# Kernel optimization log

Measured on AMD Instinct MI355X. Metric: run time of the kernel, lower is better.

Reference implementation:

```python
import jax, jax.numpy as jnp
import numpy as np

N_NODES = 50000
N_EDGES = 800000
IN_FT = 128
HID_FT = 64
EMB_FT = 128
NUM_LAYERS = 4
NEG_SLOP = 0.2


def setup_inputs() -> dict:
    key = jax.random.key(0)
    ks = jax.random.split(key, 16)
    x = jax.random.normal(ks[0], (N_NODES, IN_FT), dtype=jnp.float32)
    edge_index = jax.random.randint(ks[1], (2, N_EDGES), 0, N_NODES, dtype=jnp.int64)
    edge_weight = jax.random.uniform(ks[2], (N_EDGES,), dtype=jnp.float32)
    def lin(k, fin, fout):
        s = 1.0 / np.sqrt(fin)
        kw, kb = jax.random.split(k)
        W = jax.random.uniform(kw, (fin, fout), minval=-s, maxval=s, dtype=jnp.float32)
        b = jax.random.uniform(kb, (fout,), minval=-s, maxval=s, dtype=jnp.float32)
        return W, b
    W1, b1 = lin(ks[3], IN_FT, HID_FT)
    W2, b2 = lin(ks[4], HID_FT, HID_FT)
    W3, b3 = lin(ks[5], HID_FT, HID_FT)
    W4, b4 = lin(ks[6], HID_FT, HID_FT)
    Wh, bh = lin(ks[7], NUM_LAYERS * HID_FT, EMB_FT)
    return {"x": x, "edge_index": edge_index, "edge_weight": edge_weight,
            "W1": W1, "b1": b1, "W2": W2, "b2": b2, "W3": W3, "b3": b3,
            "W4": W4, "b4": b4, "Wh": Wh, "bh": bh}


def _gcn_no_norm(x, src, dst, ew, W, b):
    # GCNConv(add_self_loops=False, normalize=False): plain weighted scatter-add
    h = x @ W                                   # [N, F]
    msg = h[src] * ew[:, None]                  # gather over edges [E, F]
    return jax.ops.segment_sum(msg, dst, num_segments=N_NODES) + b


def _gcn_norm(x, src, dst, ew, W, b):
    # Default GCNConv: add self loops (weight 1) + symmetric normalization.
    deg = jax.ops.segment_sum(ew, dst, num_segments=N_NODES) + 1.0  # +1 self loop
    dinv = jnp.where(deg > 0, jax.lax.rsqrt(deg), 0.0)
    norm = dinv[src] * ew * dinv[dst]           # [E]
    h = x @ W
    agg = jax.ops.segment_sum(h[src] * norm[:, None], dst, num_segments=N_NODES)
    agg = agg + (dinv * dinv)[:, None] * h      # self-loop term
    return agg + b


def _forward(x, edge_index, edge_weight, W1, b1, W2, b2, W3, b3, W4, b4, Wh, bh):
    src, dst = edge_index[0], edge_index[1]
    lrelu = lambda v: jax.nn.leaky_relu(v, NEG_SLOP)
    outs = []
    h = lrelu(_gcn_no_norm(x, src, dst, edge_weight, W1, b1))
    outs.append(h)  # dropout is identity in deterministic reference
    for W, b in ((W2, b2), (W3, b3), (W4, b4)):
        h = lrelu(_gcn_norm(h, src, dst, edge_weight, W, b))
        outs.append(h)
    cat = jnp.concatenate(outs, axis=-1)        # [N, num_layers*HID_FT]
    return cat @ Wh + bh


def reference(x, edge_index, edge_weight, W1, b1, W2, b2, W3, b3, W4, b4, Wh, bh):
    return _forward(x, edge_index, edge_weight, W1, b1, W2, b2, W3, b3, W4, b4, Wh, bh)
```

## Files before the change

### kernel.cpp

```cpp
#include <hip/hip_runtime.h>
#include <hip/hip_bf16.h>

#define NEG_SLOP 0.2f
typedef unsigned long long ull;
typedef __attribute__((ext_vector_type(8))) short bf16x8;
typedef __attribute__((ext_vector_type(4))) float f32x4;

__device__ __forceinline__ float lrelu(float v) { return v > 0.0f ? v : NEG_SLOP * v; }

__device__ __forceinline__ float bf2f(unsigned short u) {
    union { unsigned int i; float f; } c; c.i = ((unsigned int)u) << 16; return c.f;
}
__device__ __forceinline__ unsigned short f2bf(float f) {
    union { float f; unsigned int i; } c; c.f = f;
    unsigned int r = c.i + 0x7FFF + ((c.i >> 16) & 1);
    return (unsigned short)(r >> 16);
}

__global__ void histo_kernel(const int* __restrict__ dst, const float* __restrict__ ew,
                             ull* __restrict__ packed, int* __restrict__ rank, int n_edges) {
    int e = blockIdx.x * 256 + threadIdx.x;
    if (e >= n_edges) return;
    int d = dst[e];
    ull delta = (1ULL << 40) | (ull)(ew[e] * 4294967296.0f);
    ull old = atomicAdd(&packed[d], delta);
    rank[e] = (int)(old >> 40);
}

__global__ void dinv_kernel(const ull* __restrict__ packed, float* __restrict__ dinv, int n) {
    int i = blockIdx.x * 256 + threadIdx.x;
    if (i >= n) return;
    float deg = (float)(packed[i] & ((1ULL << 40) - 1)) * (1.0f / 4294967296.0f);
    dinv[i] = rsqrtf(deg + 1.0f);
}

__global__ void scan1_kernel(const ull* __restrict__ packed, int* __restrict__ pre,
                             int* __restrict__ bsum, int n) {
    __shared__ int s[256];
    int t = threadIdx.x;
    int base = blockIdx.x * 1024 + t * 4;
    int c[4];
#pragma unroll
    for (int j = 0; j < 4; ++j) c[j] = (base + j < n) ? (int)(packed[base + j] >> 40) : 0;
    int tsum = c[0] + c[1] + c[2] + c[3];
    s[t] = tsum;
    __syncthreads();
    for (int off = 1; off < 256; off <<= 1) {
        int v = (t >= off) ? s[t - off] : 0;
        __syncthreads();
        s[t] += v;
        __syncthreads();
    }
    int ex = s[t] - tsum;
    if (t == 255) bsum[blockIdx.x] = s[255];
    int o[4];
    o[0] = ex; o[1] = ex + c[0]; o[2] = o[1] + c[1]; o[3] = o[2] + c[2];
    if (base + 3 < n) *(int4*)&pre[base] = make_int4(o[0], o[1], o[2], o[3]);
    else {
        for (int j = 0; j < 4; ++j) if (base + j < n) pre[base + j] = o[j];
    }
}

__global__ void scan2_kernel(int* __restrict__ bsum, int nb) {
    __shared__ int s[64];
    int t = threadIdx.x;
    int v = (t < nb) ? bsum[t] : 0;
    s[t] = v;
    __syncthreads();
    for (int off = 1; off < 64; off <<= 1) {
        int u = (t >= off) ? s[t - off] : 0;
        __syncthreads();
        s[t] += u;
        __syncthreads();
    }
    if (t < nb) bsum[t] = s[t] - v;
}

__global__ void scan3_kernel(int* __restrict__ rp, const int* __restrict__ bsum,
                             int n, int n_edges) {
    int t = blockIdx.x * 256 + threadIdx.x;
    int base = t * 4;
    if (base >= n) {
        if (base == ((n + 3) & ~3)) rp[n] = n_edges;
        return;
    }
    int boff = bsum[base >> 10];
    if (base + 3 < n) {
        int4 v = *(const int4*)&rp[base];
        v.x += boff; v.y += boff; v.z += boff; v.w += boff;
        *(int4*)&rp[base] = v;
    } else {
        for (int j = 0; j < 4 && base + j < n; ++j) rp[base + j] += boff;
        rp[n] = n_edges;
    }
}

__global__ void fill_kernel(const int* __restrict__ src, const int* __restrict__ dst,
                            const float* __restrict__ ew, const int* __restrict__ rank,
                            const int* __restrict__ rp, int2* __restrict__ e_sw, int n_edges) {
    int e = blockIdx.x * 256 + threadIdx.x;
    if (e >= n_edges) return;
    int pos = rp[dst[e]] + rank[e];
    e_sw[pos] = make_int2(src[e], __float_as_int(ew[e]));
}

__global__ void gather_plain(const int* __restrict__ rp, const int2* __restrict__ e_sw,
                             const unsigned short* __restrict__ hb,
                             const float* __restrict__ b, unsigned short* __restrict__ cat, int n) {
    int node = (blockIdx.x * 256 + threadIdx.x) >> 6;
    if (node >= n) return;
    int lane = threadIdx.x & 63;
    int eg = lane >> 4;
    int f0 = (lane & 15) * 4;
    int lo = rp[node], hi = rp[node + 1];
    float a0 = 0.f, a1 = 0.f, a2 = 0.f, a3 = 0.f;
    for (int k = lo + eg; k < hi; k += 16) {
        int k1 = k + 4, k2 = k + 8, k3 = k + 12;
        int2 p0 = e_sw[k];
        int2 p1 = e_sw[k1 < hi ? k1 : k];
        int2 p2 = e_sw[k2 < hi ? k2 : k];
        int2 p3 = e_sw[k3 < hi ? k3 : k];
        float w0 = __int_as_float(p0.y);
        float w1 = k1 < hi ? __int_as_float(p1.y) : 0.f;
        float w2 = k2 < hi ? __int_as_float(p2.y) : 0.f;
        float w3 = k3 < hi ? __int_as_float(p3.y) : 0.f;
        ushort4 u0 = *(const ushort4*)&hb[(size_t)p0.x * 64 + f0];
        ushort4 u1 = *(const ushort4*)&hb[(size_t)p1.x * 64 + f0];
        ushort4 u2 = *(const ushort4*)&hb[(size_t)p2.x * 64 + f0];
        ushort4 u3 = *(const ushort4*)&hb[(size_t)p3.x * 64 + f0];
        a0 += w0 * bf2f(u0.x) + w1 * bf2f(u1.x) + w2 * bf2f(u2.x) + w3 * bf2f(u3.x);
        a1 += w0 * bf2f(u0.y) + w1 * bf2f(u1.y) + w2 * bf2f(u2.y) + w3 * bf2f(u3.y);
        a2 += w0 * bf2f(u0.z) + w1 * bf2f(u1.z) + w2 * bf2f(u2.z) + w3 * bf2f(u3.z);
        a3 += w0 * bf2f(u0.w) + w1 * bf2f(u1.w) + w2 * bf2f(u2.w) + w3 * bf2f(u3.w);
    }
    a0 += __shfl_xor(a0, 16, 64); a0 += __shfl_xor(a0, 32, 64);
    a1 += __shfl_xor(a1, 16, 64); a1 += __shfl_xor(a1, 32, 64);
    a2 += __shfl_xor(a2, 16, 64); a2 += __shfl_xor(a2, 32, 64);
    a3 += __shfl_xor(a3, 16, 64); a3 += __shfl_xor(a3, 32, 64);
    if (eg == 0) {
        ushort4 o;
        o.x = f2bf(lrelu(a0 + b[f0 + 0])); o.y = f2bf(lrelu(a1 + b[f0 + 1]));
        o.z = f2bf(lrelu(a2 + b[f0 + 2])); o.w = f2bf(lrelu(a3 + b[f0 + 3]));
        *(ushort4*)&cat[(size_t)node * 256 + f0] = o;
    }
}

__global__ void gather_norm(const int* __restrict__ rp, const int2* __restrict__ e_sw,
                            const unsigned short* __restrict__ hb,
                            const float* __restrict__ dinv, const float* __restrict__ b,
                            unsigned short* __restrict__ cat, int col_off, int n) {
    int node = (blockIdx.x * 256 + threadIdx.x) >> 6;
    if (node >= n) return;
    int lane = threadIdx.x & 63;
    int eg = lane >> 4;
    int f0 = (lane & 15) * 4;
    int lo = rp[node], hi = rp[node + 1];
    float a0 = 0.f, a1 = 0.f, a2 = 0.f, a3 = 0.f;
    for (int k = lo + eg; k < hi; k += 16) {
        int k1 = k + 4, k2 = k + 8, k3 = k + 12;
        int2 p0 = e_sw[k];
        int2 p1 = e_sw[k1 < hi ? k1 : k];
        int2 p2 = e_sw[k2 < hi ? k2 : k];
        int2 p3 = e_sw[k3 < hi ? k3 : k];
        float w0 = __int_as_float(p0.y);
        float w1 = k1 < hi ? __int_as_float(p1.y) : 0.f;
        float w2 = k2 < hi ? __int_as_float(p2.y) : 0.f;
        float w3 = k3 < hi ? __int_as_float(p3.y) : 0.f;
        ushort4 u0 = *(const ushort4*)&hb[(size_t)p0.x * 64 + f0];
        ushort4 u1 = *(const ushort4*)&hb[(size_t)p1.x * 64 + f0];
        ushort4 u2 = *(const ushort4*)&hb[(size_t)p2.x * 64 + f0];
        ushort4 u3 = *(const ushort4*)&hb[(size_t)p3.x * 64 + f0];
        a0 += w0 * bf2f(u0.x) + w1 * bf2f(u1.x) + w2 * bf2f(u2.x) + w3 * bf2f(u3.x);
        a1 += w0 * bf2f(u0.y) + w1 * bf2f(u1.y) + w2 * bf2f(u2.y) + w3 * bf2f(u3.y);
        a2 += w0 * bf2f(u0.z) + w1 * bf2f(u1.z) + w2 * bf2f(u2.z) + w3 * bf2f(u3.z);
        a3 += w0 * bf2f(u0.w) + w1 * bf2f(u1.w) + w2 * bf2f(u2.w) + w3 * bf2f(u3.w);
    }
    a0 += __shfl_xor(a0, 16, 64); a0 += __shfl_xor(a0, 32, 64);
    a1 += __shfl_xor(a1, 16, 64); a1 += __shfl_xor(a1, 32, 64);
    a2 += __shfl_xor(a2, 16, 64); a2 += __shfl_xor(a2, 32, 64);
    a3 += __shfl_xor(a3, 16, 64); a3 += __shfl_xor(a3, 32, 64);
    if (eg == 0) {
        float di = dinv[node];
        ushort4 h = *(const ushort4*)&hb[(size_t)node * 64 + f0];
        ushort4 o;
        o.x = f2bf(lrelu(di * (a0 + bf2f(h.x)) + b[f0 + 0]));
        o.y = f2bf(lrelu(di * (a1 + bf2f(h.y)) + b[f0 + 1]));
        o.z = f2bf(lrelu(di * (a2 + bf2f(h.z)) + b[f0 + 2]));
        o.w = f2bf(lrelu(di * (a3 + bf2f(h.w)) + b[f0 + 3]));
        *(ushort4*)&cat[(size_t)node * 256 + col_off + f0] = o;
    }
}

__global__ __launch_bounds__(256) void gemm_hid_f32(
    const float* __restrict__ in, int in_stride, int K,
    const float* __restrict__ W, unsigned short* __restrict__ outb, int n_rows) {
    __shared__ float Ws[64 * 64];
    __shared__ float XsT[64 * 132];
    const int tid = threadIdx.x;
    const int tc = tid & 15, tr = tid >> 4;
    const int row0 = blockIdx.x * 128;
    float acc[8][4] = {};
    for (int kc = 0; kc < K; kc += 64) {
        __syncthreads();
        for (int i = tid; i < 64 * 64; i += 256) Ws[i] = W[kc * 64 + i];
        {
            int k = tid & 63, rq = tid >> 6;
            for (int i = 0; i < 32; ++i) {
                int r = rq * 32 + i;
                int rr = row0 + r; if (rr >= n_rows) rr = n_rows - 1;
                XsT[k * 132 + r] = in[(size_t)rr * in_stride + kc + k];
            }
        }
        __syncthreads();
        for (int kk = 0; kk < 64; ++kk) {
            float4 w4 = *(const float4*)&Ws[kk * 64 + tc * 4];
            float4 aA = *(const float4*)&XsT[kk * 132 + tr * 8];
            float4 aB = *(const float4*)&XsT[kk * 132 + tr * 8 + 4];
            float a[8] = {aA.x, aA.y, aA.z, aA.w, aB.x, aB.y, aB.z, aB.w};
#pragma unroll
            for (int i = 0; i < 8; ++i) {
                acc[i][0] += a[i] * w4.x; acc[i][1] += a[i] * w4.y;
                acc[i][2] += a[i] * w4.z; acc[i][3] += a[i] * w4.w;
            }
        }
    }
#pragma unroll
    for (int i = 0; i < 8; ++i) {
        int r = row0 + tr * 8 + i;
        if (r >= n_rows) break;
        ushort4 o;
        o.x = f2bf(acc[i][0]); o.y = f2bf(acc[i][1]);
        o.z = f2bf(acc[i][2]); o.w = f2bf(acc[i][3]);
        *(ushort4*)&outb[(size_t)r * 64 + tc * 4] = o;
    }
}

__global__ __launch_bounds__(256) void gemm_hid_b(
    const unsigned short* __restrict__ in, int in_stride,
    const float* __restrict__ W, const float* __restrict__ dinv,
    unsigned short* __restrict__ outb, int n_rows) {
    __shared__ float Ws[64 * 64];
    __shared__ float XsT[64 * 132];
    const int tid = threadIdx.x;
    const int tc = tid & 15, tr = tid >> 4;
    const int row0 = blockIdx.x * 128;
    float acc[8][4] = {};
    for (int i = tid; i < 64 * 64; i += 256) Ws[i] = W[i];
    {
        int k2 = tid & 31, rq = tid >> 5;
        for (int i = 0; i < 16; ++i) {
            int r = rq * 16 + i;
            int rr = row0 + r; if (rr >= n_rows) rr = n_rows - 1;
            ushort2 u = *(const ushort2*)&in[(size_t)rr * in_stride + 2 * k2];
            XsT[(2 * k2) * 132 + r] = bf2f(u.x);
            XsT[(2 * k2 + 1) * 132 + r] = bf2f(u.y);
        }
    }
    __syncthreads();
    for (int kk = 0; kk < 64; ++kk) {
        float4 w4 = *(const float4*)&Ws[kk * 64 + tc * 4];
        float4 aA = *(const float4*)&XsT[kk * 132 + tr * 8];
        float4 aB = *(const float4*)&XsT[kk * 132 + tr * 8 + 4];
        float a[8] = {aA.x, aA.y, aA.z, aA.w, aB.x, aB.y, aB.z, aB.w};
#pragma unroll
        for (int i = 0; i < 8; ++i) {
            acc[i][0] += a[i] * w4.x; acc[i][1] += a[i] * w4.y;
            acc[i][2] += a[i] * w4.z; acc[i][3] += a[i] * w4.w;
        }
    }
#pragma unroll
    for (int i = 0; i < 8; ++i) {
        int r = row0 + tr * 8 + i;
        if (r >= n_rows) break;
        float di = dinv[r];
        ushort4 o;
        o.x = f2bf(acc[i][0] * di); o.y = f2bf(acc[i][1] * di);
        o.z = f2bf(acc[i][2] * di); o.w = f2bf(acc[i][3] * di);
        *(ushort4*)&outb[(size_t)r * 64 + tc * 4] = o;
    }
}

__global__ void wht_kernel(const float* __restrict__ Wh, unsigned short* __restrict__ wht) {
    int idx = blockIdx.x * 256 + threadIdx.x;
    if (idx >= 256 * 128) return;
    int k = idx >> 7, c = idx & 127;
    wht[(size_t)c * 256 + k] = f2bf(Wh[idx]);
}

__global__ __launch_bounds__(256) void gemm_out_mfma(
    const unsigned short* __restrict__ cat, const unsigned short* __restrict__ whT,
    const float* __restrict__ bh, float* __restrict__ out, int n_rows) {
    __shared__ __align__(16) char As[64 * 128];
    __shared__ __align__(16) char Bs[128 * 128];
    const int tid = threadIdx.x;
    const int wid = tid >> 6, lane = tid & 63;
    const int row0 = blockIdx.x * 64;
    const int lrow = lane & 15, kg = lane >> 4;
    f32x4 acc[8] = {};
    for (int kc = 0; kc < 4; ++kc) {
        __syncthreads();
        {
            int row = tid >> 2, seg = tid & 3;
            int rr = row0 + row; if (rr >= n_rows) rr = n_rows - 1;
            const int4* g = (const int4*)&cat[(size_t)rr * 256 + kc * 64 + seg * 16];
            int4 u0 = g[0], u1 = g[1];
            int sw = (row & 7) << 4;
            int base = row * 128 + seg * 32;
            *(int4*)(As + (base ^ sw)) = u0;
            *(int4*)(As + ((base + 16) ^ sw)) = u1;
        }
        {
            int c = tid >> 1, seg = tid & 1;
            const int4* g = (const int4*)&whT[(size_t)c * 256 + kc * 64 + seg * 32];
            int sw = (c & 7) << 4;
            int base = c * 128 + seg * 64;
#pragma unroll
            for (int i = 0; i < 4; ++i)
                *(int4*)(Bs + ((base + i * 16) ^ sw)) = g[i];
        }
        __syncthreads();
        int arow = wid * 16 + lrow;
        int asw = (arow & 7) << 4;
#pragma unroll
        for (int ks = 0; ks < 2; ++ks) {
            bf16x8 af = *(bf16x8*)(As + ((arow * 128 + ks * 64 + kg * 16) ^ asw));
#pragma unroll
            for (int cf = 0; cf < 8; ++cf) {
                int c = cf * 16 + lrow;
                bf16x8 bf = *(bf16x8*)(Bs + ((c * 128 + ks * 64 + kg * 16) ^ ((c & 7) << 4)));
                acc[cf] = __builtin_amdgcn_mfma_f32_16x16x32_bf16(af, bf, acc[cf], 0, 0, 0);
            }
        }
    }
    int lrow4 = (lane >> 4) * 4;
#pragma unroll
    for (int cf = 0; cf < 8; ++cf) {
        int col = cf * 16 + lrow;
        float bias = bh[col];
#pragma unroll
        for (int reg = 0; reg < 4; ++reg) {
            int r = row0 + wid * 16 + lrow4 + reg;
            if (r < n_rows) out[(size_t)r * 128 + col] = acc[cf][reg] + bias;
        }
    }
}

extern "C" void kernel_launch(void* const* d_in, const int* in_sizes, int n_in,
                              void* d_out, int out_size, void* d_ws, size_t ws_size,
                              hipStream_t stream) {
    const float* x  = (const float*)d_in[0];
    const int*   ei = (const int*)d_in[1];
    const float* ew = (const float*)d_in[2];
    const float* W1 = (const float*)d_in[3];
    const float* b1 = (const float*)d_in[4];
    const float* W2 = (const float*)d_in[5];
    const float* b2 = (const float*)d_in[6];
    const float* W3 = (const float*)d_in[7];
    const float* b3 = (const float*)d_in[8];
    const float* W4 = (const float*)d_in[9];
    const float* b4 = (const float*)d_in[10];
    const float* Wh = (const float*)d_in[11];
    const float* bh = (const float*)d_in[12];

    const int E = in_sizes[2];
    const int N = in_sizes[0] / 128;
    const int* src = ei;
    const int* dst = ei + E;

    char* p = (char*)d_ws;
    unsigned short* cat     = (unsigned short*)p; p += (size_t)N * 256 * 2;
    unsigned short* hb      = (unsigned short*)p; p += (size_t)N * 64 * 2;
    unsigned short* wht     = (unsigned short*)p; p += (size_t)128 * 256 * 2;
    ull*            packed  = (ull*)p;            p += (size_t)N * 8;
    float*          dinv    = (float*)p;          p += (size_t)N * 4;
    int*            row_ptr = (int*)p;            p += (size_t)(N + 4) * 4;
    int*            bsum    = (int*)p;            p += (size_t)64 * 4;
    int*            rank    = (int*)p;            p += (size_t)E * 4;
    int2*           e_sw    = (int2*)p;           p += (size_t)E * 8;
    float* out = (float*)d_out;

    int eb   = (E + 255) / 256;
    int nb   = (N + 255) / 256;
    int nb64 = (N * 64 + 255) / 256;
    int gb   = (N + 127) / 128;
    int gb64 = (N + 63) / 64;
    int sb   = (N + 1023) / 1024;
    int s3b  = ((N + 3) / 4 + 256) / 256;

    hipMemsetAsync(packed, 0, (size_t)N * 8, stream);
    wht_kernel<<<128, 256, 0, stream>>>(Wh, wht);
    histo_kernel<<<eb, 256, 0, stream>>>(dst, ew, packed, rank, E);
    dinv_kernel<<<nb, 256, 0, stream>>>(packed, dinv, N);
    scan1_kernel<<<sb, 256, 0, stream>>>(packed, row_ptr, bsum, N);
    scan2_kernel<<<1, 64, 0, stream>>>(bsum, sb);
    scan3_kernel<<<s3b, 256, 0, stream>>>(row_ptr, bsum, N, E);
    fill_kernel<<<eb, 256, 0, stream>>>(src, dst, ew, rank, row_ptr, e_sw, E);

    gemm_hid_f32<<<gb, 256, 0, stream>>>(x, 128, 128, W1, hb, N);
    gather_plain<<<nb64, 256, 0, stream>>>(row_ptr, e_sw, hb, b1, cat, N);

    const float* Wl[3] = {W2, W3, W4};
    const float* bl[3] = {b2, b3, b4};
    for (int l = 1; l < 4; ++l) {
        gemm_hid_b<<<gb, 256, 0, stream>>>(cat + (size_t)(l - 1) * 64, 256, Wl[l - 1],
                                           dinv, hb, N);
        gather_norm<<<nb64, 256, 0, stream>>>(row_ptr, e_sw, hb, dinv,
                                              bl[l - 1], cat, l * 64, N);
    }

    gemm_out_mfma<<<gb64, 256, 0, stream>>>(cat, wht, bh, out, N);
}
```

Baseline: 257.5 us.

## Split degree histogram atomics into four sub-counters and fuse memset with Wh transpose

The per-node packed count/weight atomic counter is replicated four ways, indexed by edge id mod 4, to reduce atomic contention in the histogram pass. The dinv and scan kernels sum the four copies, and a new per-node int4 of sub-bases lets the fill kernel compute each edge's CSR slot. The memset of the counters is folded into the Wh transpose kernel to remove one launch. The cost is four times the counter memory plus an extra per-node bases array that has to be written and then read.

```diff
diff --git a/kernel.cpp b/kernel.cpp
--- a/kernel.cpp
+++ b/kernel.cpp
@@ -17,32 +17,57 @@
     return (unsigned short)(r >> 16);
 }
 
+__global__ void prep_kernel(const float* __restrict__ Wh, unsigned short* __restrict__ wht,
+                            float4* __restrict__ pz, int nz) {
+    int idx = blockIdx.x * 256 + threadIdx.x;
+    if (idx < nz) pz[idx] = make_float4(0.f, 0.f, 0.f, 0.f);
+    if (idx < 256 * 128) {
+        int k = idx >> 7, c = idx & 127;
+        wht[(size_t)c * 256 + k] = f2bf(Wh[idx]);
+    }
+}
+
 __global__ void histo_kernel(const int* __restrict__ dst, const float* __restrict__ ew,
-                             ull* __restrict__ packed, int* __restrict__ rank, int n_edges) {
+                             ull* __restrict__ packed4, int* __restrict__ rank,
+                             int n_edges, int n) {
     int e = blockIdx.x * 256 + threadIdx.x;
     if (e >= n_edges) return;
     int d = dst[e];
+    int c = e & 3;
     ull delta = (1ULL << 40) | (ull)(ew[e] * 4294967296.0f);
-    ull old = atomicAdd(&packed[d], delta);
+    ull old = atomicAdd(&packed4[(size_t)c * n + d], delta);
     rank[e] = (int)(old >> 40);
 }
 
-__global__ void dinv_kernel(const ull* __restrict__ packed, float* __restrict__ dinv, int n) {
+__global__ void dinv_kernel(const ull* __restrict__ packed4, float* __restrict__ dinv, int n) {
     int i = blockIdx.x * 256 + threadIdx.x;
     if (i >= n) return;
-    float deg = (float)(packed[i] & ((1ULL << 40) - 1)) * (1.0f / 4294967296.0f);
+    const ull m = (1ULL << 40) - 1;
+    ull s = (packed4[i] & m) + (packed4[(size_t)n + i] & m) +
+            (packed4[2 * (size_t)n + i] & m) + (packed4[3 * (size_t)n + i] & m);
+    float deg = (float)s * (1.0f / 4294967296.0f);
     dinv[i] = rsqrtf(deg + 1.0f);
 }
 
-__global__ void scan1_kernel(const ull* __restrict__ packed, int* __restrict__ pre,
-                             int* __restrict__ bsum, int n) {
+__global__ void scan1_kernel(const ull* __restrict__ packed4, int* __restrict__ pre,
+                             int4* __restrict__ bases, int* __restrict__ bsum, int n) {
     __shared__ int s[256];
     int t = threadIdx.x;
     int base = blockIdx.x * 1024 + t * 4;
-    int c[4];
-#pragma unroll
-    for (int j = 0; j < 4; ++j) c[j] = (base + j < n) ? (int)(packed[base + j] >> 40) : 0;
-    int tsum = c[0] + c[1] + c[2] + c[3];
+    int tot[4];
+#pragma unroll
+    for (int j = 0; j < 4; ++j) {
+        int node = base + j;
+        if (node < n) {
+            int c0 = (int)(packed4[node] >> 40);
+            int c1 = (int)(packed4[(size_t)n + node] >> 40);
+            int c2 = (int)(packed4[2 * (size_t)n + node] >> 40);
+            int c3 = (int)(packed4[3 * (size_t)n + node] >> 40);
+            bases[node] = make_int4(0, c0, c0 + c1, c0 + c1 + c2);
+            tot[j] = c0 + c1 + c2 + c3;
+        } else tot[j] = 0;
+    }
+    int tsum = tot[0] + tot[1] + tot[2] + tot[3];
     s[t] = tsum;
     __syncthreads();
     for (int off = 1; off < 256; off <<= 1) {
@@ -54,7 +79,7 @@
     int ex = s[t] - tsum;
     if (t == 255) bsum[blockIdx.x] = s[255];
     int o[4];
-    o[0] = ex; o[1] = ex + c[0]; o[2] = o[1] + c[1]; o[3] = o[2] + c[2];
+    o[0] = ex; o[1] = ex + tot[0]; o[2] = o[1] + tot[1]; o[3] = o[2] + tot[2];
     if (base + 3 < n) *(int4*)&pre[base] = make_int4(o[0], o[1], o[2], o[3]);
     else {
         for (int j = 0; j < 4; ++j) if (base + j < n) pre[base + j] = o[j];
@@ -97,10 +122,15 @@
 
 __global__ void fill_kernel(const int* __restrict__ src, const int* __restrict__ dst,
                             const float* __restrict__ ew, const int* __restrict__ rank,
-                            const int* __restrict__ rp, int2* __restrict__ e_sw, int n_edges) {
+                            const int* __restrict__ rp, const int4* __restrict__ bases,
+                            int2* __restrict__ e_sw, int n_edges) {
     int e = blockIdx.x * 256 + threadIdx.x;
     if (e >= n_edges) return;
-    int pos = rp[dst[e]] + rank[e];
+    int d = dst[e];
+    int c = e & 3;
+    int4 bs = bases[d];
+    int b = (c == 0) ? bs.x : (c == 1) ? bs.y : (c == 2) ? bs.z : bs.w;
+    int pos = rp[d] + b + rank[e];
     e_sw[pos] = make_int2(src[e], __float_as_int(ew[e]));
 }
 
@@ -280,13 +310,6 @@
     }
 }
 
-__global__ void wht_kernel(const float* __restrict__ Wh, unsigned short* __restrict__ wht) {
-    int idx = blockIdx.x * 256 + threadIdx.x;
-    if (idx >= 256 * 128) return;
-    int k = idx >> 7, c = idx & 127;
-    wht[(size_t)c * 256 + k] = f2bf(Wh[idx]);
-}
-
 __global__ __launch_bounds__(256) void gemm_out_mfma(
     const unsigned short* __restrict__ cat, const unsigned short* __restrict__ whT,
     const float* __restrict__ bh, float* __restrict__ out, int n_rows) {
@@ -371,10 +394,11 @@
     unsigned short* cat     = (unsigned short*)p; p += (size_t)N * 256 * 2;
     unsigned short* hb      = (unsigned short*)p; p += (size_t)N * 64 * 2;
     unsigned short* wht     = (unsigned short*)p; p += (size_t)128 * 256 * 2;
-    ull*            packed  = (ull*)p;            p += (size_t)N * 8;
+    ull*            packed4 = (ull*)p;            p += (size_t)N * 4 * 8;
     float*          dinv    = (float*)p;          p += (size_t)N * 4;
     int*            row_ptr = (int*)p;            p += (size_t)(N + 4) * 4;
     int*            bsum    = (int*)p;            p += (size_t)64 * 4;
+    int4*           bases   = (int4*)p;           p += (size_t)N * 16;
     int*            rank    = (int*)p;            p += (size_t)E * 4;
     int2*           e_sw    = (int2*)p;           p += (size_t)E * 8;
     float* out = (float*)d_out;
@@ -386,15 +410,16 @@
     int gb64 = (N + 63) / 64;
     int sb   = (N + 1023) / 1024;
     int s3b  = ((N + 3) / 4 + 256) / 256;
-
-    hipMemsetAsync(packed, 0, (size_t)N * 8, stream);
-    wht_kernel<<<128, 256, 0, stream>>>(Wh, wht);
-    histo_kernel<<<eb, 256, 0, stream>>>(dst, ew, packed, rank, E);
-    dinv_kernel<<<nb, 256, 0, stream>>>(packed, dinv, N);
-    scan1_kernel<<<sb, 256, 0, stream>>>(packed, row_ptr, bsum, N);
+    int nz   = N * 2;
+    int pb   = (nz > 256 * 128 ? nz : 256 * 128) / 256 + 1;
+
+    prep_kernel<<<pb, 256, 0, stream>>>(Wh, wht, (float4*)packed4, nz);
+    histo_kernel<<<eb, 256, 0, stream>>>(dst, ew, packed4, rank, E, N);
+    dinv_kernel<<<nb, 256, 0, stream>>>(packed4, dinv, N);
+    scan1_kernel<<<sb, 256, 0, stream>>>(packed4, row_ptr, bases, bsum, N);
     scan2_kernel<<<1, 64, 0, stream>>>(bsum, sb);
     scan3_kernel<<<s3b, 256, 0, stream>>>(row_ptr, bsum, N, E);
-    fill_kernel<<<eb, 256, 0, stream>>>(src, dst, ew, rank, row_ptr, e_sw, E);
+    fill_kernel<<<eb, 256, 0, stream>>>(src, dst, ew, rank, row_ptr, bases, e_sw, E);
 
     gemm_hid_f32<<<gb, 256, 0, stream>>>(x, 128, 128, W1, hb, N);
     gather_plain<<<nb64, 256, 0, stream>>>(row_ptr, e_sw, hb, b1, cat, N);
```

Result: no change. 259.7 us (+0.8%).
